# Kernel optimization log

Measured on AMD Instinct MI355X. Metric: run time of the kernel, lower is better.

Reference implementation:

```python
import jax, jax.numpy as jnp
import numpy as np

N = 50000      # nodes
E = 800000     # edges
C = 128        # in channels
H = 128        # hidden1 = hidden2 = hidden3
B = 256        # graphs in batch
CLS = 10       # classes
MLP_H = 64
EPS = 1e-5


def _lin_params(key, fan_in, fan_out):
    k1, k2 = jax.random.split(key)
    s = 1.0 / np.sqrt(fan_in)
    W = jax.random.uniform(k1, (fan_in, fan_out), jnp.float32, -s, s)
    b = jax.random.uniform(k2, (fan_out,), jnp.float32, -s, s)
    return W, b


def setup_inputs() -> dict:
    key = jax.random.key(0)
    ks = jax.random.split(key, 10)
    x = jax.random.normal(ks[0], (N, C), jnp.float32)
    edge_index = jax.random.randint(ks[1], (2, E), 0, N)
    edge_attr = jax.random.uniform(ks[2], (E,), jnp.float32)
    batch = jnp.sort(jax.random.randint(ks[3], (N,), 0, B))
    W1, b1 = _lin_params(ks[4], C, H)
    W2, b2 = _lin_params(ks[5], H, H)
    W3, b3 = _lin_params(ks[6], H, H)
    gamma = jnp.ones((H,), jnp.float32)
    beta = jnp.zeros((H,), jnp.float32)
    Wm1, bm1 = _lin_params(ks[7], H, MLP_H)
    Wm2, bm2 = _lin_params(ks[8], MLP_H, CLS)
    return dict(x=x, edge_index=edge_index, edge_attr=edge_attr, batch=batch,
                W1=W1, b1=b1, W2=W2, b2=b2, W3=W3, b3=b3,
                gamma=gamma, beta=beta, Wm1=Wm1, bm1=bm1, Wm2=Wm2, bm2=bm2)


def gcn_conv(x, src, dst, ew, W, b):
    # PyG GCNConv: linear (no bias) -> gcn_norm with self-loops -> scatter-add -> +bias
    h = x @ W                                                  # [N, out]
    deg = jax.ops.segment_sum(ew, dst, num_segments=N) + 1.0   # self-loop weight 1
    dinv = jnp.where(deg > 0, jax.lax.rsqrt(deg), 0.0)
    norm = dinv[src] * ew * dinv[dst]                          # [E]
    agg = jax.ops.segment_sum(norm[:, None] * h[src], dst, num_segments=N)
    agg = agg + h * (dinv * dinv)[:, None]                     # self-loop messages
    return agg + b


def reference(x, edge_index, edge_attr, batch,
              W1, b1, W2, b2, W3, b3, gamma, beta, Wm1, bm1, Wm2, bm2):
    src, dst = edge_index[0], edge_index[1]
    ew = edge_attr.reshape(-1)
    h = jax.nn.relu(gcn_conv(x, src, dst, ew, W1, b1))
    h = jax.nn.relu(gcn_conv(h, src, dst, ew, W2, b2))
    h = jax.nn.relu(gcn_conv(h, src, dst, ew, W3, b3))
    # BatchNorm (training-mode batch stats, biased variance)
    mu = jnp.mean(h, axis=0)
    var = jnp.mean((h - mu) ** 2, axis=0)
    h = (h - mu) * jax.lax.rsqrt(var + EPS) * gamma + beta
    # global_mean_pool over graph ids
    counts = jax.ops.segment_sum(jnp.ones((N,), jnp.float32), batch, num_segments=B)
    g = jax.ops.segment_sum(h, batch, num_segments=B) / jnp.maximum(counts, 1.0)[:, None]
    # MLP head (two stacked linears, no activation between)
    pred = (g @ Wm1 + bm1) @ Wm2 + bm2
    return pred
```

## Files before the change

kernel.cpp:

```cpp
#include <hip/hip_runtime.h>
#include <hip/hip_bf16.h>

#define NN 50000
#define EE 800000
#define HH 128
#define BB 256
#define CLS 10
#define MLPH 64
#define CAP 64

#define NBUK 196
#define NBLK 250
#define EPB 3200
#define SCAN_N (NBUK * NBLK)
#define SCAN_BLKS 192

typedef __attribute__((ext_vector_type(8))) short short8;
typedef __attribute__((ext_vector_type(4))) float floatx4;

__device__ __forceinline__ float bflo(unsigned u){ unsigned v = u << 16; return __builtin_bit_cast(float, v); }
__device__ __forceinline__ float bfhi(unsigned u){ unsigned v = u & 0xffff0000u; return __builtin_bit_cast(float, v); }
__device__ __forceinline__ unsigned short f2bf(float f){
  unsigned u = __builtin_bit_cast(unsigned, f);
  u += 0x7fffu + ((u >> 16) & 1u);
  return (unsigned short)(u >> 16);
}
__device__ __forceinline__ unsigned pack2(float a, float b){
  return (unsigned)f2bf(a) | ((unsigned)f2bf(b) << 16);
}

__global__ __launch_bounds__(256) void bin_count_k(const int* __restrict__ dst, int* __restrict__ cnts){
  __shared__ int hist[NBUK];
  int t = threadIdx.x, blk = blockIdx.x;
  if (t < NBUK) hist[t] = 0;
  __syncthreads();
  int e0 = blk * EPB;
  #pragma unroll 4
  for (int i = 0; i < 12; ++i) atomicAdd(&hist[dst[e0 + i * 256 + t] >> 8], 1);
  if (t < 128) atomicAdd(&hist[dst[e0 + 3072 + t] >> 8], 1);
  __syncthreads();
  if (t < NBUK) cnts[t * NBLK + blk] = hist[t];
}

__global__ __launch_bounds__(256) void scanA_k(int* data, int* bsum){
  __shared__ int sd[256];
  int t = threadIdx.x;
  int i = blockIdx.x * 256 + t;
  int v = (i < SCAN_N) ? data[i] : 0;
  sd[t] = v; __syncthreads();
  for (int off = 1; off < 256; off <<= 1){
    int add = (t >= off) ? sd[t - off] : 0;
    __syncthreads();
    sd[t] += add;
    __syncthreads();
  }
  if (i < SCAN_N) data[i] = sd[t] - v;
  if (t == 255) bsum[blockIdx.x] = sd[255];
}
__global__ __launch_bounds__(256) void scanB_k(int* bsum){
  __shared__ int sd[256];
  int t = threadIdx.x;
  int v = (t < SCAN_BLKS) ? bsum[t] : 0;
  sd[t] = v; __syncthreads();
  for (int off = 1; off < 256; off <<= 1){
    int add = (t >= off) ? sd[t - off] : 0;
    __syncthreads();
    sd[t] += add;
    __syncthreads();
  }
  if (t < SCAN_BLKS) bsum[t] = sd[t] - v;
}

__global__ __launch_bounds__(256) void bin_scatter_k(const int* __restrict__ src, const int* __restrict__ dst,
                                                     const float* __restrict__ ew,
                                                     const int* __restrict__ sc, const int* __restrict__ bsum,
                                                     int2* __restrict__ ebin){
  __shared__ int lbase[NBUK];
  __shared__ int lrank[NBUK];
  int t = threadIdx.x, blk = blockIdx.x;
  if (t < NBUK){
    int idx = t * NBLK + blk;
    lbase[t] = sc[idx] + bsum[idx >> 8];
    lrank[t] = 0;
  }
  __syncthreads();
  int e0 = blk * EPB;
  for (int i = 0; i < 13; ++i){
    int off = i * 256 + t;
    if (off < EPB){
      int e = e0 + off;
      int d = dst[e];
      int u = d >> 8;
      int r = atomicAdd(&lrank[u], 1);
      int2 rec; rec.x = src[e] | ((d & 255) << 16); rec.y = __builtin_bit_cast(int, ew[e]);
      ebin[lbase[u] + r] = rec;
    }
  }
}

__global__ __launch_bounds__(256) void bucket_sort_k(const int2* __restrict__ ebin, const int* __restrict__ sc,
                                                     const int* __restrict__ bsum,
                                                     unsigned* __restrict__ ebuf, int* __restrict__ cnt,
                                                     float* __restrict__ dinv){
  __shared__ int hist[256];
  __shared__ float wsum[256];
  int t = threadIdx.x, u = blockIdx.x;
  hist[t] = 0; wsum[t] = 0.0f;
  __syncthreads();
  int i0 = u * NBLK;
  int s0 = sc[i0] + bsum[i0 >> 8];
  int s1 = EE;
  if (u + 1 < NBUK){ int i1 = (u + 1) * NBLK; s1 = sc[i1] + bsum[i1 >> 8]; }
  for (int e = s0 + t; e < s1; e += 256){
    int2 rec = ebin[e];
    int dl = rec.x >> 16;
    float w = __builtin_bit_cast(float, rec.y);
    int r = atomicAdd(&hist[dl], 1);
    atomicAdd(&wsum[dl], w);
    if (r < CAP){
      unsigned c4 = (unsigned)(rec.x & 0xFFFF) | ((unsigned)f2bf(w) << 16);
      ebuf[((size_t)(u * 256 + dl)) * CAP + r] = c4;
    }
  }
  __syncthreads();
  int n = u * 256 + t;
  if (n < NN){
    cnt[n] = min(hist[t], CAP);
    dinv[n] = rsqrtf(1.0f + wsum[t]);
  }
}

__global__ __launch_bounds__(256) void gbounds_k(const int* __restrict__ batch, int* gstart,
                                                 float* bnsum, float* bnsqs){
  int b = threadIdx.x;
  if (b < HH){ bnsum[b] = 0.0f; bnsqs[b] = 0.0f; }
  int lo = 0, hi = NN;
  while (lo < hi){
    int mid = (lo + hi) >> 1;
    if (batch[mid] < b) lo = mid + 1; else hi = mid;
  }
  gstart[b] = lo;
  if (b == 0) gstart[BB] = NN;
}

__global__ __launch_bounds__(256) void transpose3_k(const float* W1, const float* W2, const float* W3,
                                                    unsigned short* Wt1, unsigned short* Wt2, unsigned short* Wt3){
  int gi = blockIdx.x * 256 + threadIdx.x;
  int w = gi >> 14;
  int i = gi & 16383;
  const float* W = (w == 0) ? W1 : (w == 1) ? W2 : W3;
  unsigned short* Wt = (w == 0) ? Wt1 : (w == 1) ? Wt2 : Wt3;
  int n = i >> 7, k = i & 127;
  Wt[i] = f2bf(W[(k << 7) + n]);
}

__global__ __launch_bounds__(256) void gemm128_k(const unsigned short* __restrict__ X,
                                                 const unsigned short* __restrict__ Wt,
                                                 const float* __restrict__ dinv,
                                                 unsigned short* __restrict__ Gout, int nrows){
  __shared__ __align__(16) unsigned short lw[HH * 136];
  {
    const float4* s4 = (const float4*)Wt;
    float4* d4 = (float4*)lw;
    for (int i = threadIdx.x; i < 2048; i += 256){
      int row = i >> 4, off = i & 15;
      d4[row * 17 + off] = s4[i];
    }
  }
  __syncthreads();
  int wave = threadIdx.x >> 6;
  int lane = threadIdx.x & 63;
  int r16 = lane & 15, quad = lane >> 4;
  int m0 = blockIdx.x * 128 + wave * 32;

  short8 xfrag[2][4];
  float dv[2];
  for (int nt = 0; nt < 2; ++nt){
    int m = m0 + nt * 16 + r16;
    int msafe = (m < nrows) ? m : 0;
    const short8* xrow = (const short8*)(X + (size_t)msafe * HH);
    for (int kk = 0; kk < 4; ++kk) xfrag[nt][kk] = xrow[4 * kk + quad];
    dv[nt] = (m < nrows) ? dinv[m] : 0.0f;
  }
  for (int ct = 0; ct < 8; ++ct){
    floatx4 acc0 = {0.f,0.f,0.f,0.f}, acc1 = {0.f,0.f,0.f,0.f};
    const short8* wrow = (const short8*)(lw + (16 * ct + r16) * 136);
    for (int kk = 0; kk < 4; ++kk){
      short8 wfrag = wrow[4 * kk + quad];
      acc0 = __builtin_amdgcn_mfma_f32_16x16x32_bf16(wfrag, xfrag[0][kk], acc0, 0, 0, 0);
      acc1 = __builtin_amdgcn_mfma_f32_16x16x32_bf16(wfrag, xfrag[1][kk], acc1, 0, 0, 0);
    }
    int ch0 = ct * 16 + quad * 4;
    int m = m0 + r16;
    if (m < nrows){
      uint2 pk; pk.x = pack2(acc0[0] * dv[0], acc0[1] * dv[0]);
      pk.y = pack2(acc0[2] * dv[0], acc0[3] * dv[0]);
      ((uint2*)Gout)[((size_t)m * HH + ch0) >> 2] = pk;
    }
    int m2 = m0 + 16 + r16;
    if (m2 < nrows){
      uint2 pk; pk.x = pack2(acc1[0] * dv[1], acc1[1] * dv[1]);
      pk.y = pack2(acc1[2] * dv[1], acc1[3] * dv[1]);
      ((uint2*)Gout)[((size_t)m2 * HH + ch0) >> 2] = pk;
    }
  }
}

__global__ __launch_bounds__(256) void gemm128_f32_k(const float* __restrict__ X,
                                                     const unsigned short* __restrict__ Wt,
                                                     const float* __restrict__ dinv,
                                                     unsigned short* __restrict__ Gout, int nrows){
  __shared__ __align__(16) unsigned short lw[HH * 136];
  {
    const float4* s4 = (const float4*)Wt;
    float4* d4 = (float4*)lw;
    for (int i = threadIdx.x; i < 2048; i += 256){
      int row = i >> 4, off = i & 15;
      d4[row * 17 + off] = s4[i];
    }
  }
  __syncthreads();
  int wave = threadIdx.x >> 6;
  int lane = threadIdx.x & 63;
  int r16 = lane & 15, quad = lane >> 4;
  int m0 = blockIdx.x * 128 + wave * 32;

  short8 xfrag[2][4];
  float dv[2];
  for (int nt = 0; nt < 2; ++nt){
    int m = m0 + nt * 16 + r16;
    int msafe = (m < nrows) ? m : 0;
    const float4* xr = (const float4*)(X + (size_t)msafe * HH);
    for (int kk = 0; kk < 4; ++kk){
      float4 aA = xr[kk * 8 + quad * 2];
      float4 aB = xr[kk * 8 + quad * 2 + 1];
      uint4 pk;
      pk.x = pack2(aA.x, aA.y); pk.y = pack2(aA.z, aA.w);
      pk.z = pack2(aB.x, aB.y); pk.w = pack2(aB.z, aB.w);
      xfrag[nt][kk] = __builtin_bit_cast(short8, pk);
    }
    dv[nt] = (m < nrows) ? dinv[m] : 0.0f;
  }
  for (int ct = 0; ct < 8; ++ct){
    floatx4 acc0 = {0.f,0.f,0.f,0.f}, acc1 = {0.f,0.f,0.f,0.f};
    const short8* wrow = (const short8*)(lw + (16 * ct + r16) * 136);
    for (int kk = 0; kk < 4; ++kk){
      short8 wfrag = wrow[4 * kk + quad];
      acc0 = __builtin_amdgcn_mfma_f32_16x16x32_bf16(wfrag, xfrag[0][kk], acc0, 0, 0, 0);
      acc1 = __builtin_amdgcn_mfma_f32_16x16x32_bf16(wfrag, xfrag[1][kk], acc1, 0, 0, 0);
    }
    int ch0 = ct * 16 + quad * 4;
    int m = m0 + r16;
    if (m < nrows){
      uint2 pk; pk.x = pack2(acc0[0] * dv[0], acc0[1] * dv[0]);
      pk.y = pack2(acc0[2] * dv[0], acc0[3] * dv[0]);
      ((uint2*)Gout)[((size_t)m * HH + ch0) >> 2] = pk;
    }
    int m2 = m0 + 16 + r16;
    if (m2 < nrows){
      uint2 pk; pk.x = pack2(acc1[0] * dv[1], acc1[1] * dv[1]);
      pk.y = pack2(acc1[2] * dv[1], acc1[3] * dv[1]);
      ((uint2*)Gout)[((size_t)m2 * HH + ch0) >> 2] = pk;
    }
  }
}

__global__ __launch_bounds__(256) void aggregate_k(const unsigned short* __restrict__ Gin,
                                                   const unsigned* __restrict__ ebuf,
                                                   const int* __restrict__ cnt,
                                                   const float* __restrict__ dinv,
                                                   const float* __restrict__ bias,
                                                   unsigned short* __restrict__ Xout){
  __shared__ float part[4][4][16][8];
  int wv = threadIdx.x >> 6, lane = threadIdx.x & 63;
  int node = blockIdx.x * 4 + wv;
  int g = lane >> 4, l = lane & 15;
  int c = min(cnt[node], CAP);
  unsigned rec = 0;
  if (lane < c) rec = ebuf[(size_t)node * CAP + lane];
  float acc[8] = {0,0,0,0,0,0,0,0};
  const uint4* G4 = (const uint4*)Gin;
  int steps = (c + 3) >> 2;
  #pragma unroll 4
  for (int j = 0; j < steps; ++j){
    int idx = 4 * j + g;
    unsigned r = (unsigned)__shfl((int)rec, idx);
    int sx = r & 0xFFFF;
    float w = bfhi(r);
    if (idx >= c){ sx = 0; w = 0.0f; }
    uint4 q = G4[(size_t)sx * 16 + l];
    acc[0] = fmaf(w, bflo(q.x), acc[0]);
    acc[1] = fmaf(w, bfhi(q.x), acc[1]);
    acc[2] = fmaf(w, bflo(q.y), acc[2]);
    acc[3] = fmaf(w, bfhi(q.y), acc[3]);
    acc[4] = fmaf(w, bflo(q.z), acc[4]);
    acc[5] = fmaf(w, bfhi(q.z), acc[5]);
    acc[6] = fmaf(w, bflo(q.w), acc[6]);
    acc[7] = fmaf(w, bfhi(q.w), acc[7]);
  }
  #pragma unroll
  for (int k = 0; k < 8; ++k) part[wv][g][l][k] = acc[k];
  __syncthreads();
  int l0 = lane >> 2, k0 = (lane & 3) * 2;
  float a0 = part[wv][0][l0][k0]   + part[wv][1][l0][k0]   + part[wv][2][l0][k0]   + part[wv][3][l0][k0];
  float a1 = part[wv][0][l0][k0+1] + part[wv][1][l0][k0+1] + part[wv][2][l0][k0+1] + part[wv][3][l0][k0+1];
  unsigned gs = ((const unsigned*)Gin)[(size_t)node * 64 + lane];
  a0 += bflo(gs); a1 += bfhi(gs);
  float di = dinv[node];
  float2 bb = ((const float2*)bias)[lane];
  a0 = fmaxf(fmaf(di, a0, bb.x), 0.0f);
  a1 = fmaxf(fmaf(di, a1, bb.y), 0.0f);
  ((unsigned*)Xout)[(size_t)node * 64 + lane] = pack2(a0, a1);
}

__global__ __launch_bounds__(256) void pool_k(const unsigned short* __restrict__ H3,
                                              const int* __restrict__ gstart,
                                              float* __restrict__ S, float* bnsum, float* bnsqs,
                                              float* cntf){
  __shared__ float rs0[256], rs1[256], rq0[256], rq1[256];
  int b = blockIdx.x;
  int t = threadIdx.x, colc = t & 63, sub = t >> 6;
  int start = gstart[b], end = gstart[b + 1];
  const unsigned* Hrow = (const unsigned*)H3;
  float s0 = 0, s1 = 0, q0 = 0, q1 = 0;
  #pragma unroll 4
  for (int n = start + sub; n < end; n += 4){
    unsigned h = Hrow[(size_t)n * 64 + colc];
    float a = bflo(h), c = bfhi(h);
    s0 += a; s1 += c; q0 += a * a; q1 += c * c;
  }
  rs0[t] = s0; rs1[t] = s1; rq0[t] = q0; rq1[t] = q1;
  __syncthreads();
  if (sub == 0){
    float t0 = rs0[colc] + rs0[colc + 64] + rs0[colc + 128] + rs0[colc + 192];
    float t1 = rs1[colc] + rs1[colc + 64] + rs1[colc + 128] + rs1[colc + 192];
    float u0 = rq0[colc] + rq0[colc + 64] + rq0[colc + 128] + rq0[colc + 192];
    float u1 = rq1[colc] + rq1[colc + 64] + rq1[colc + 128] + rq1[colc + 192];
    S[b * HH + 2 * colc]     = t0;
    S[b * HH + 2 * colc + 1] = t1;
    atomicAdd(&bnsum[2 * colc], t0);
    atomicAdd(&bnsum[2 * colc + 1], t1);
    atomicAdd(&bnsqs[2 * colc], u0);
    atomicAdd(&bnsqs[2 * colc + 1], u1);
    if (t == 0) cntf[b] = (float)(end - start);
  }
}

__global__ __launch_bounds__(64) void mlp_head_k(const float* __restrict__ S, const float* __restrict__ cntf,
                                                 const float* __restrict__ bnsum, const float* __restrict__ bnsqs,
                                                 const float* gamma, const float* beta,
                                                 const float* Wm1, const float* bm1,
                                                 const float* Wm2, const float* bm2,
                                                 float* out){
  __shared__ float gb[HH];
  __shared__ float t[MLPH];
  int b = blockIdx.x, j = threadIdx.x;
  float inv = 1.0f / fmaxf(cntf[b], 1.0f);
  for (int c = j; c < HH; c += 64){
    float mu = bnsum[c] * (1.0f / NN);
    float var = bnsqs[c] * (1.0f / NN) - mu * mu;
    float istd = rsqrtf(var + 1e-5f);
    float g = S[b * HH + c] * inv;
    gb[c] = (g - mu) * istd * gamma[c] + beta[c];
  }
  __syncthreads();
  float acc = bm1[j];
  for (int k = 0; k < HH; ++k) acc = fmaf(gb[k], Wm1[k * MLPH + j], acc);
  t[j] = acc;
  __syncthreads();
  if (j < CLS){
    float o = bm2[j];
    for (int k = 0; k < MLPH; ++k) o = fmaf(t[k], Wm2[k * CLS + j], o);
    out[b * CLS + j] = o;
  }
}

static inline size_t al(size_t x){ return (x + 255) & ~(size_t)255; }

extern "C" void kernel_launch(void* const* d_in, const int* in_sizes, int n_in,
                              void* d_out, int out_size, void* d_ws, size_t ws_size,
                              hipStream_t stream){
  const float* x     = (const float*)d_in[0];
  const int*   ei    = (const int*)d_in[1];
  const float* ea    = (const float*)d_in[2];
  const int*   batch = (const int*)d_in[3];
  const float* W1 = (const float*)d_in[4];
  const float* b1 = (const float*)d_in[5];
  const float* W2 = (const float*)d_in[6];
  const float* b2 = (const float*)d_in[7];
  const float* W3 = (const float*)d_in[8];
  const float* b3 = (const float*)d_in[9];
  const float* gamma = (const float*)d_in[10];
  const float* beta  = (const float*)d_in[11];
  const float* Wm1 = (const float*)d_in[12];
  const float* bm1 = (const float*)d_in[13];
  const float* Wm2 = (const float*)d_in[14];
  const float* bm2 = (const float*)d_in[15];
  const int* srcv = ei;
  const int* dstv = ei + EE;

  char* p = (char*)d_ws;
  float* dinv   = (float*)p;            p += al(NN * 4);
  int*   cnt    = (int*)p;              p += al(NN * 4);
  int*   cnts   = (int*)p;              p += al((size_t)SCAN_N * 4);
  int*   bsum   = (int*)p;              p += al(SCAN_BLKS * 4);
  int*   gstart = (int*)p;              p += al((BB + 1) * 4);
  int2*  ebin   = (int2*)p;             p += al((size_t)EE * 8);
  unsigned* ebuf = (unsigned*)p;        p += al((size_t)NN * CAP * 4);
  unsigned short* Wt1  = (unsigned short*)p; p += al(HH * HH * 2);
  unsigned short* Wt2  = (unsigned short*)p; p += al(HH * HH * 2);
  unsigned short* Wt3  = (unsigned short*)p; p += al(HH * HH * 2);
  unsigned short* bufA = (unsigned short*)p; p += al((size_t)NN * HH * 2);
  unsigned short* bufB = (unsigned short*)p; p += al((size_t)NN * HH * 2);
  float* S     = (float*)p;             p += al(BB * HH * 4);
  float* bnsum = (float*)p;             p += al(HH * 4);
  float* bnsqs = (float*)p;             p += al(HH * 4);
  float* cntf  = (float*)p;             p += al(BB * 4);

  const int nT = 256;
  dim3 gW((NN + 3) / 4);

  bin_count_k<<<dim3(NBLK), nT, 0, stream>>>(dstv, cnts);
  scanA_k<<<dim3(SCAN_BLKS), nT, 0, stream>>>(cnts, bsum);
  scanB_k<<<dim3(1), nT, 0, stream>>>(bsum);
  bin_scatter_k<<<dim3(NBLK), nT, 0, stream>>>(srcv, dstv, ea, cnts, bsum, ebin);
  bucket_sort_k<<<dim3(NBUK), nT, 0, stream>>>(ebin, cnts, bsum, ebuf, cnt, dinv);
  gbounds_k<<<dim3(1), nT, 0, stream>>>(batch, gstart, bnsum, bnsqs);
  transpose3_k<<<dim3(192), nT, 0, stream>>>(W1, W2, W3, Wt1, Wt2, Wt3);

  dim3 gGemm((NN + 127) / 128);
  gemm128_f32_k<<<gGemm, nT, 0, stream>>>(x, Wt1, dinv, bufA, NN);
  aggregate_k<<<gW, nT, 0, stream>>>(bufA, ebuf, cnt, dinv, b1, bufB);
  gemm128_k<<<gGemm, nT, 0, stream>>>(bufB, Wt2, dinv, bufA, NN);
  aggregate_k<<<gW, nT, 0, stream>>>(bufA, ebuf, cnt, dinv, b2, bufB);
  gemm128_k<<<gGemm, nT, 0, stream>>>(bufB, Wt3, dinv, bufA, NN);
  aggregate_k<<<gW, nT, 0, stream>>>(bufA, ebuf, cnt, dinv, b3, bufB);

  pool_k<<<dim3(BB), nT, 0, stream>>>(bufB, gstart, S, bnsum, bnsqs, cntf);
  mlp_head_k<<<dim3(BB), dim3(64), 0, stream>>>(S, cntf, bnsum, bnsqs, gamma, beta,
                                                Wm1, bm1, Wm2, bm2, (float*)d_out);
}
```

Measured before the change: 286.9 us.

## Use finer 64-node buckets, smaller GEMM tiles, and merge prep kernels

```diff
diff --git a/kernel.cpp b/kernel.cpp
--- a/kernel.cpp
+++ b/kernel.cpp
@@ -9,11 +9,11 @@
 #define MLPH 64
 #define CAP 64
 
-#define NBUK 196
+#define NBUK 782
 #define NBLK 250
 #define EPB 3200
 #define SCAN_N (NBUK * NBLK)
-#define SCAN_BLKS 192
+#define SCAN_BLKS 764
 
 typedef __attribute__((ext_vector_type(8))) short short8;
 typedef __attribute__((ext_vector_type(4))) float floatx4;
@@ -32,14 +32,14 @@
 __global__ __launch_bounds__(256) void bin_count_k(const int* __restrict__ dst, int* __restrict__ cnts){
   __shared__ int hist[NBUK];
   int t = threadIdx.x, blk = blockIdx.x;
-  if (t < NBUK) hist[t] = 0;
+  for (int i = t; i < NBUK; i += 256) hist[i] = 0;
   __syncthreads();
   int e0 = blk * EPB;
   #pragma unroll 4
-  for (int i = 0; i < 12; ++i) atomicAdd(&hist[dst[e0 + i * 256 + t] >> 8], 1);
-  if (t < 128) atomicAdd(&hist[dst[e0 + 3072 + t] >> 8], 1);
-  __syncthreads();
-  if (t < NBUK) cnts[t * NBLK + blk] = hist[t];
+  for (int i = 0; i < 12; ++i) atomicAdd(&hist[dst[e0 + i * 256 + t] >> 6], 1);
+  if (t < 128) atomicAdd(&hist[dst[e0 + 3072 + t] >> 6], 1);
+  __syncthreads();
+  for (int u = t; u < NBUK; u += 256) cnts[u * NBLK + blk] = hist[u];
 }
 
 __global__ __launch_bounds__(256) void scanA_k(int* data, int* bsum){
@@ -59,16 +59,25 @@
 }
 __global__ __launch_bounds__(256) void scanB_k(int* bsum){
   __shared__ int sd[256];
+  __shared__ int carry;
   int t = threadIdx.x;
-  int v = (t < SCAN_BLKS) ? bsum[t] : 0;
-  sd[t] = v; __syncthreads();
-  for (int off = 1; off < 256; off <<= 1){
-    int add = (t >= off) ? sd[t - off] : 0;
+  if (t == 0) carry = 0;
+  __syncthreads();
+  for (int c = 0; c < 3; ++c){
+    int i = c * 256 + t;
+    int v = (i < SCAN_BLKS) ? bsum[i] : 0;
+    sd[t] = v; __syncthreads();
+    for (int off = 1; off < 256; off <<= 1){
+      int add = (t >= off) ? sd[t - off] : 0;
+      __syncthreads();
+      sd[t] += add;
+      __syncthreads();
+    }
+    if (i < SCAN_BLKS) bsum[i] = carry + sd[t] - v;
     __syncthreads();
-    sd[t] += add;
+    if (t == 255) carry += sd[255];
     __syncthreads();
   }
-  if (t < SCAN_BLKS) bsum[t] = sd[t] - v;
 }
 
 __global__ __launch_bounds__(256) void bin_scatter_k(const int* __restrict__ src, const int* __restrict__ dst,
@@ -78,10 +87,10 @@
   __shared__ int lbase[NBUK];
   __shared__ int lrank[NBUK];
   int t = threadIdx.x, blk = blockIdx.x;
-  if (t < NBUK){
-    int idx = t * NBLK + blk;
-    lbase[t] = sc[idx] + bsum[idx >> 8];
-    lrank[t] = 0;
+  for (int i = t; i < NBUK; i += 256){
+    int idx = i * NBLK + blk;
+    lbase[i] = sc[idx] + bsum[idx >> 8];
+    lrank[i] = 0;
   }
   __syncthreads();
   int e0 = blk * EPB;
@@ -90,9 +99,9 @@
     if (off < EPB){
       int e = e0 + off;
       int d = dst[e];
-      int u = d >> 8;
+      int u = d >> 6;
       int r = atomicAdd(&lrank[u], 1);
-      int2 rec; rec.x = src[e] | ((d & 255) << 16); rec.y = __builtin_bit_cast(int, ew[e]);
+      int2 rec; rec.x = src[e] | ((d & 63) << 16); rec.y = __builtin_bit_cast(int, ew[e]);
       ebin[lbase[u] + r] = rec;
     }
   }
@@ -102,10 +111,10 @@
                                                      const int* __restrict__ bsum,
                                                      unsigned* __restrict__ ebuf, int* __restrict__ cnt,
                                                      float* __restrict__ dinv){
-  __shared__ int hist[256];
-  __shared__ float wsum[256];
+  __shared__ int hist[64];
+  __shared__ float wsum[64];
   int t = threadIdx.x, u = blockIdx.x;
-  hist[t] = 0; wsum[t] = 0.0f;
+  if (t < 64){ hist[t] = 0; wsum[t] = 0.0f; }
   __syncthreads();
   int i0 = u * NBLK;
   int s0 = sc[i0] + bsum[i0 >> 8];
@@ -119,33 +128,37 @@
     atomicAdd(&wsum[dl], w);
     if (r < CAP){
       unsigned c4 = (unsigned)(rec.x & 0xFFFF) | ((unsigned)f2bf(w) << 16);
-      ebuf[((size_t)(u * 256 + dl)) * CAP + r] = c4;
-    }
-  }
-  __syncthreads();
-  int n = u * 256 + t;
-  if (n < NN){
-    cnt[n] = min(hist[t], CAP);
-    dinv[n] = rsqrtf(1.0f + wsum[t]);
-  }
-}
-
-__global__ __launch_bounds__(256) void gbounds_k(const int* __restrict__ batch, int* gstart,
-                                                 float* bnsum, float* bnsqs){
-  int b = threadIdx.x;
-  if (b < HH){ bnsum[b] = 0.0f; bnsqs[b] = 0.0f; }
-  int lo = 0, hi = NN;
-  while (lo < hi){
-    int mid = (lo + hi) >> 1;
-    if (batch[mid] < b) lo = mid + 1; else hi = mid;
-  }
-  gstart[b] = lo;
-  if (b == 0) gstart[BB] = NN;
-}
-
-__global__ __launch_bounds__(256) void transpose3_k(const float* W1, const float* W2, const float* W3,
-                                                    unsigned short* Wt1, unsigned short* Wt2, unsigned short* Wt3){
-  int gi = blockIdx.x * 256 + threadIdx.x;
+      ebuf[((size_t)(u * 64 + dl)) * CAP + r] = c4;
+    }
+  }
+  __syncthreads();
+  if (t < 64){
+    int n = u * 64 + t;
+    if (n < NN){
+      cnt[n] = min(hist[t], CAP);
+      dinv[n] = rsqrtf(1.0f + wsum[t]);
+    }
+  }
+}
+
+__global__ __launch_bounds__(256) void prep_k(const float* W1, const float* W2, const float* W3,
+                                              unsigned short* Wt1, unsigned short* Wt2, unsigned short* Wt3,
+                                              const int* __restrict__ batch, int* gstart,
+                                              float* bnsum, float* bnsqs){
+  int blk = blockIdx.x, t = threadIdx.x;
+  if (blk == 192){
+    int b = t;
+    if (b < HH){ bnsum[b] = 0.0f; bnsqs[b] = 0.0f; }
+    int lo = 0, hi = NN;
+    while (lo < hi){
+      int mid = (lo + hi) >> 1;
+      if (batch[mid] < b) lo = mid + 1; else hi = mid;
+    }
+    gstart[b] = lo;
+    if (b == 0) gstart[BB] = NN;
+    return;
+  }
+  int gi = blk * 256 + t;
   int w = gi >> 14;
   int i = gi & 16383;
   const float* W = (w == 0) ? W1 : (w == 1) ? W2 : W3;
@@ -154,10 +167,10 @@
   Wt[i] = f2bf(W[(k << 7) + n]);
 }
 
-__global__ __launch_bounds__(256) void gemm128_k(const unsigned short* __restrict__ X,
-                                                 const unsigned short* __restrict__ Wt,
-                                                 const float* __restrict__ dinv,
-                                                 unsigned short* __restrict__ Gout, int nrows){
+__global__ __launch_bounds__(256) void gemm64_k(const unsigned short* __restrict__ X,
+                                                const unsigned short* __restrict__ Wt,
+                                                const float* __restrict__ dinv,
+                                                unsigned short* __restrict__ Gout, int nrows){
   __shared__ __align__(16) unsigned short lw[HH * 136];
   {
     const float4* s4 = (const float4*)Wt;
@@ -171,45 +184,35 @@
   int wave = threadIdx.x >> 6;
   int lane = threadIdx.x & 63;
   int r16 = lane & 15, quad = lane >> 4;
-  int m0 = blockIdx.x * 128 + wave * 32;
-
-  short8 xfrag[2][4];
-  float dv[2];
-  for (int nt = 0; nt < 2; ++nt){
-    int m = m0 + nt * 16 + r16;
-    int msafe = (m < nrows) ? m : 0;
-    const short8* xrow = (const short8*)(X + (size_t)msafe * HH);
-    for (int kk = 0; kk < 4; ++kk) xfrag[nt][kk] = xrow[4 * kk + quad];
-    dv[nt] = (m < nrows) ? dinv[m] : 0.0f;
-  }
+  int m = blockIdx.x * 64 + wave * 16 + r16;
+
+  short8 xfrag[4];
+  int msafe = (m < nrows) ? m : 0;
+  const short8* xrow = (const short8*)(X + (size_t)msafe * HH);
+  #pragma unroll
+  for (int kk = 0; kk < 4; ++kk) xfrag[kk] = xrow[4 * kk + quad];
+  float dv = (m < nrows) ? dinv[m] : 0.0f;
+
+  #pragma unroll
   for (int ct = 0; ct < 8; ++ct){
-    floatx4 acc0 = {0.f,0.f,0.f,0.f}, acc1 = {0.f,0.f,0.f,0.f};
+    floatx4 acc = {0.f,0.f,0.f,0.f};
     const short8* wrow = (const short8*)(lw + (16 * ct + r16) * 136);
-    for (int kk = 0; kk < 4; ++kk){
-      short8 wfrag = wrow[4 * kk + quad];
-      acc0 = __builtin_amdgcn_mfma_f32_16x16x32_bf16(wfrag, xfrag[0][kk], acc0, 0, 0, 0);
-      acc1 = __builtin_amdgcn_mfma_f32_16x16x32_bf16(wfrag, xfrag[1][kk], acc1, 0, 0, 0);
-    }
+    #pragma unroll
+    for (int kk = 0; kk < 4; ++kk)
+      acc = __builtin_amdgcn_mfma_f32_16x16x32_bf16(wrow[4 * kk + quad], xfrag[kk], acc, 0, 0, 0);
     int ch0 = ct * 16 + quad * 4;
-    int m = m0 + r16;
     if (m < nrows){
-      uint2 pk; pk.x = pack2(acc0[0] * dv[0], acc0[1] * dv[0]);
-      pk.y = pack2(acc0[2] * dv[0], acc0[3] * dv[0]);
+      uint2 pk; pk.x = pack2(acc[0] * dv, acc[1] * dv);
+      pk.y = pack2(acc[2] * dv, acc[3] * dv);
       ((uint2*)Gout)[((size_t)m * HH + ch0) >> 2] = pk;
     }
-    int m2 = m0 + 16 + r16;
-    if (m2 < nrows){
-      uint2 pk; pk.x = pack2(acc1[0] * dv[1], acc1[1] * dv[1]);
-      pk.y = pack2(acc1[2] * dv[1], acc1[3] * dv[1]);
-      ((uint2*)Gout)[((size_t)m2 * HH + ch0) >> 2] = pk;
-    }
-  }
-}
-
-__global__ __launch_bounds__(256) void gemm128_f32_k(const float* __restrict__ X,
-                                                     const unsigned short* __restrict__ Wt,
-                                                     const float* __restrict__ dinv,
-                                                     unsigned short* __restrict__ Gout, int nrows){
+  }
+}
+
+__global__ __launch_bounds__(256) void gemm64_f32_k(const float* __restrict__ X,
+                                                    const unsigned short* __restrict__ Wt,
+                                                    const float* __restrict__ dinv,
+                                                    unsigned short* __restrict__ Gout, int nrows){
   __shared__ __align__(16) unsigned short lw[HH * 136];
   {
     const float4* s4 = (const float4*)Wt;
@@ -223,44 +226,34 @@
   int wave = threadIdx.x >> 6;
   int lane = threadIdx.x & 63;
   int r16 = lane & 15, quad = lane >> 4;
-  int m0 = blockIdx.x * 128 + wave * 32;
-
-  short8 xfrag[2][4];
-  float dv[2];
-  for (int nt = 0; nt < 2; ++nt){
-    int m = m0 + nt * 16 + r16;
-    int msafe = (m < nrows) ? m : 0;
-    const float4* xr = (const float4*)(X + (size_t)msafe * HH);
-    for (int kk = 0; kk < 4; ++kk){
-      float4 aA = xr[kk * 8 + quad * 2];
-      float4 aB = xr[kk * 8 + quad * 2 + 1];
-      uint4 pk;
-      pk.x = pack2(aA.x, aA.y); pk.y = pack2(aA.z, aA.w);
-      pk.z = pack2(aB.x, aB.y); pk.w = pack2(aB.z, aB.w);
-      xfrag[nt][kk] = __builtin_bit_cast(short8, pk);
-    }
-    dv[nt] = (m < nrows) ? dinv[m] : 0.0f;
-  }
+  int m = blockIdx.x * 64 + wave * 16 + r16;
+
+  short8 xfrag[4];
+  int msafe = (m < nrows) ? m : 0;
+  const float4* xr = (const float4*)(X + (size_t)msafe * HH);
+  #pragma unroll
+  for (int kk = 0; kk < 4; ++kk){
+    float4 aA = xr[kk * 8 + quad * 2];
+    float4 aB = xr[kk * 8 + quad * 2 + 1];
+    uint4 pk;
+    pk.x = pack2(aA.x, aA.y); pk.y = pack2(aA.z, aA.w);
+    pk.z = pack2(aB.x, aB.y); pk.w = pack2(aB.z, aB.w);
+    xfrag[kk] = __builtin_bit_cast(short8, pk);
+  }
+  float dv = (m < nrows) ? dinv[m] : 0.0f;
+
+  #pragma unroll
   for (int ct = 0; ct < 8; ++ct){
-    floatx4 acc0 = {0.f,0.f,0.f,0.f}, acc1 = {0.f,0.f,0.f,0.f};
+    floatx4 acc = {0.f,0.f,0.f,0.f};
     const short8* wrow = (const short8*)(lw + (16 * ct + r16) * 136);
-    for (int kk = 0; kk < 4; ++kk){
-      short8 wfrag = wrow[4 * kk + quad];
-      acc0 = __builtin_amdgcn_mfma_f32_16x16x32_bf16(wfrag, xfrag[0][kk], acc0, 0, 0, 0);
-      acc1 = __builtin_amdgcn_mfma_f32_16x16x32_bf16(wfrag, xfrag[1][kk], acc1, 0, 0, 0);
-    }
+    #pragma unroll
+    for (int kk = 0; kk < 4; ++kk)
+      acc = __builtin_amdgcn_mfma_f32_16x16x32_bf16(wrow[4 * kk + quad], xfrag[kk], acc, 0, 0, 0);
     int ch0 = ct * 16 + quad * 4;
-    int m = m0 + r16;
     if (m < nrows){
-      uint2 pk; pk.x = pack2(acc0[0] * dv[0], acc0[1] * dv[0]);
-      pk.y = pack2(acc0[2] * dv[0], acc0[3] * dv[0]);
+      uint2 pk; pk.x = pack2(acc[0] * dv, acc[1] * dv);
+      pk.y = pack2(acc[2] * dv, acc[3] * dv);
       ((uint2*)Gout)[((size_t)m * HH + ch0) >> 2] = pk;
-    }
-    int m2 = m0 + 16 + r16;
-    if (m2 < nrows){
-      uint2 pk; pk.x = pack2(acc1[0] * dv[1], acc1[1] * dv[1]);
-      pk.y = pack2(acc1[2] * dv[1], acc1[3] * dv[1]);
-      ((uint2*)Gout)[((size_t)m2 * HH + ch0) >> 2] = pk;
     }
   }
 }
@@ -425,15 +418,14 @@
   scanB_k<<<dim3(1), nT, 0, stream>>>(bsum);
   bin_scatter_k<<<dim3(NBLK), nT, 0, stream>>>(srcv, dstv, ea, cnts, bsum, ebin);
   bucket_sort_k<<<dim3(NBUK), nT, 0, stream>>>(ebin, cnts, bsum, ebuf, cnt, dinv);
-  gbounds_k<<<dim3(1), nT, 0, stream>>>(batch, gstart, bnsum, bnsqs);
-  transpose3_k<<<dim3(192), nT, 0, stream>>>(W1, W2, W3, Wt1, Wt2, Wt3);
-
-  dim3 gGemm((NN + 127) / 128);
-  gemm128_f32_k<<<gGemm, nT, 0, stream>>>(x, Wt1, dinv, bufA, NN);
+  prep_k<<<dim3(193), nT, 0, stream>>>(W1, W2, W3, Wt1, Wt2, Wt3, batch, gstart, bnsum, bnsqs);
+
+  dim3 gGemm((NN + 63) / 64);
+  gemm64_f32_k<<<gGemm, nT, 0, stream>>>(x, Wt1, dinv, bufA, NN);
   aggregate_k<<<gW, nT, 0, stream>>>(bufA, ebuf, cnt, dinv, b1, bufB);
-  gemm128_k<<<gGemm, nT, 0, stream>>>(bufB, Wt2, dinv, bufA, NN);
+  gemm64_k<<<gGemm, nT, 0, stream>>>(bufB, Wt2, dinv, bufA, NN);
   aggregate_k<<<gW, nT, 0, stream>>>(bufA, ebuf, cnt, dinv, b2, bufB);
-  gemm128_k<<<gGemm, nT, 0, stream>>>(bufB, Wt3, dinv, bufA, NN);
+  gemm64_k<<<gGemm, nT, 0, stream>>>(bufB, Wt3, dinv, bufA, NN);
   aggregate_k<<<gW, nT, 0, stream>>>(bufA, ebuf, cnt, dinv, b3, bufB);
 
   pool_k<<<dim3(BB), nT, 0, stream>>>(bufB, gstart, S, bnsum, bnsqs, cntf);
```

Measured after the change: 292.5 us. Within noise of the previous version (+2.0%).
